# Kernel optimization log

Measured on AMD Instinct MI355X. Metric: run time of the kernel, lower is better.

The kernel has to match this reference:

```python
import jax, jax.numpy as jnp
import numpy as np

TOP_K = 2


def _mlp(x, w1, b1, w2, b2):
    # Linear -> GELU -> Linear (assumed MLP body)
    h = jax.nn.gelu(jnp.einsum('bsd,di->bsi', x, w1) + b1)
    return jnp.einsum('bsi,id->bsd', h, w2) + b2


def setup_inputs() -> dict:
    key = jax.random.key(0)
    ks = jax.random.split(key, 8)
    B, S, D, I, E = 2, 2048, 1024, 4096, 8
    s_in = 1.0 / np.sqrt(D)
    s_mid = 1.0 / np.sqrt(I)
    return {
        'x': jax.random.normal(ks[0], (B, S, D), jnp.float32),
        'gate_w': jax.random.normal(ks[1], (D, E), jnp.float32) * s_in,
        'gate_b': jnp.zeros((E,), jnp.float32),
        'sh_w1': jax.random.normal(ks[2], (D, I), jnp.float32) * s_in,
        'sh_b1': jnp.zeros((I,), jnp.float32),
        'sh_w2': jax.random.normal(ks[3], (I, D), jnp.float32) * s_mid,
        'sh_b2': jnp.zeros((D,), jnp.float32),
        'ew1': jax.random.normal(ks[4], (E, D, I), jnp.float32) * s_in,
        'eb1': jnp.zeros((E, I), jnp.float32),
        'ew2': jax.random.normal(ks[5], (E, I, D), jnp.float32) * s_mid,
        'eb2': jnp.zeros((E, D), jnp.float32),
    }


def reference(x, gate_w, gate_b, sh_w1, sh_b1, sh_w2, sh_b2, ew1, eb1, ew2, eb2):
    E = ew1.shape[0]
    # Router
    router_probs = jax.nn.softmax(jnp.einsum('bsd,de->bse', x, gate_w) + gate_b, axis=-1)
    expert_values, expert_indices = jax.lax.top_k(router_probs, k=TOP_K)  # (B,S,K)
    expert_values = expert_values / (jnp.sum(expert_values, axis=-1, keepdims=True) + 1e-9)
    # Dense compute of all experts (faithful to original)
    h = jax.nn.gelu(jnp.einsum('bsd,edi->bsei', x, ew1) + eb1)  # (B,S,E,I)
    all_outputs = jnp.einsum('bsei,eid->bsed', h, ew2) + eb2    # (B,S,E,D)
    # Combine: scatter top-k weights to dense (B,S,E) then weighted sum
    one_hot = jax.nn.one_hot(expert_indices, E, dtype=x.dtype)  # (B,S,K,E)
    weights_E = (one_hot * expert_values[..., None]).sum(axis=2)  # (B,S,E)
    moe_out = jnp.einsum('bse,bsed->bsd', weights_E, all_outputs)
    return x + _mlp(x, sh_w1, sh_b1, sh_w2, sh_b2) + moe_out
```

## Files before the change

kernel.cpp:

```cpp
#include <hip/hip_runtime.h>
#include <hip/hip_bf16.h>
#include <stdint.h>

typedef short bf16x8 __attribute__((ext_vector_type(8)));
typedef float f32x4  __attribute__((ext_vector_type(4)));
typedef unsigned short u16;

#define T_TOK 4096
#define D_DIM 1024
#define I_DIM 4096
#define NE    9
#define BK    32

__device__ __forceinline__ u16 f2bf(float f) {
    union { float f; uint32_t u; } v; v.f = f;
    uint32_t u = v.u;
    u += 0x7FFFu + ((u >> 16) & 1u);
    return (u16)(u >> 16);
}

__device__ __forceinline__ float gelu_fast(float v) {
    float c2 = 1.5957691216057308f * (v + 0.044715f * v * v * v);
    return v / (1.0f + __expf(-c2));
}

__device__ __forceinline__ void gl16(const void* g, void* l) {
    __builtin_amdgcn_global_load_lds(
        (const __attribute__((address_space(1))) void*)g,
        (__attribute__((address_space(3))) void*)l, 16, 0, 0);
}

#define DSR(dst, adr, IMM) \
    asm volatile("ds_read_b128 %0, %1 offset:" #IMM : "=v"(dst) : "v"(adr) : "memory")
#define WAIT_VM(N)  asm volatile("s_waitcnt vmcnt(" #N ")" ::: "memory")
#define WAIT_LGKM() asm volatile("s_waitcnt lgkmcnt(0)" ::: "memory")

__global__ void k_init(int* counts) {
    int i = threadIdx.x;
    if (i < 16) counts[i] = (i == 8) ? T_TOK : 0;
}

__global__ __launch_bounds__(256) void k_router(
    const float* __restrict__ x, const float* __restrict__ gw,
    const float* __restrict__ gb,
    int* counts, int* lists, int* tok_e, int* tok_pos, float* tok_w)
{
    int wave = threadIdx.x >> 6, lane = threadIdx.x & 63;
    int t = blockIdx.x * 4 + wave;
    const float* xr = x + (size_t)t * D_DIM;

    float a[8];
#pragma unroll
    for (int e = 0; e < 8; ++e) a[e] = 0.f;
#pragma unroll
    for (int j = 0; j < D_DIM / 64; ++j) {
        int d = lane + 64 * j;
        float xv = xr[d];
        const float4* g = (const float4*)(gw + (size_t)d * 8);
        float4 g0 = g[0], g1 = g[1];
        a[0] += xv * g0.x; a[1] += xv * g0.y; a[2] += xv * g0.z; a[3] += xv * g0.w;
        a[4] += xv * g1.x; a[5] += xv * g1.y; a[6] += xv * g1.z; a[7] += xv * g1.w;
    }
#pragma unroll
    for (int off = 32; off >= 1; off >>= 1)
#pragma unroll
        for (int e = 0; e < 8; ++e) a[e] += __shfl_xor(a[e], off);

    float l[8];
#pragma unroll
    for (int e = 0; e < 8; ++e) l[e] = a[e] + gb[e];
    float mx = l[0];
#pragma unroll
    for (int e = 1; e < 8; ++e) mx = fmaxf(mx, l[e]);
    float p[8], Z = 0.f;
#pragma unroll
    for (int e = 0; e < 8; ++e) { p[e] = expf(l[e] - mx); Z += p[e]; }
#pragma unroll
    for (int e = 0; e < 8; ++e) p[e] /= Z;

    int e0 = 0; float v0 = p[0];
#pragma unroll
    for (int e = 1; e < 8; ++e) if (p[e] > v0) { v0 = p[e]; e0 = e; }
    int e1 = -1; float v1 = -1.f;
#pragma unroll
    for (int e = 0; e < 8; ++e) if (e != e0 && p[e] > v1) { v1 = p[e]; e1 = e; }
    float denom = v0 + v1 + 1e-9f;
    float w0 = v0 / denom, w1 = v1 / denom;

    if (lane == 0) {
        int p0 = atomicAdd(&counts[e0], 1);
        int p1 = atomicAdd(&counts[e1], 1);
        lists[e0 * T_TOK + p0] = t;
        lists[e1 * T_TOK + p1] = t;
        tok_e[2 * t] = e0;  tok_e[2 * t + 1] = e1;
        tok_pos[2 * t] = p0; tok_pos[2 * t + 1] = p1;
        tok_w[2 * t] = w0;  tok_w[2 * t + 1] = w1;
    }
}

__global__ void k_prefix(const int* counts, int* offsets) {
    if (threadIdx.x == 0) {
        int o = 0;
        for (int e = 0; e < NE; ++e) { offsets[e] = o; o += counts[e]; }
        offsets[NE] = o;
    }
}

__global__ __launch_bounds__(256) void k_castx(const float* __restrict__ x,
                                               u16* __restrict__ xb)
{
    int i = (blockIdx.x * 256 + threadIdx.x) * 8;
    float4 a = *(const float4*)(x + i), b = *(const float4*)(x + i + 4);
    u16 t[8] = { f2bf(a.x), f2bf(a.y), f2bf(a.z), f2bf(a.w),
                 f2bf(b.x), f2bf(b.y), f2bf(b.z), f2bf(b.w) };
    *(bf16x8*)&xb[i] = *(bf16x8*)t;
}

__global__ __launch_bounds__(256) void k_transcast(
    const float* __restrict__ src, u16* __restrict__ dst, int K, int N)
{
    src += (size_t)blockIdx.z * K * N;
    dst += (size_t)blockIdx.z * N * K;
    __shared__ float ls[64][33];
    int t = threadIdx.x;
    int k0 = blockIdx.y * 64, n0 = blockIdx.x * 32;
    {
        int kr = t >> 2, ng = (t & 3) * 8;
        const float* s = src + (size_t)(k0 + kr) * N + n0 + ng;
        float4 v0 = *(const float4*)s, v1 = *(const float4*)(s + 4);
        ls[kr][ng + 0] = v0.x; ls[kr][ng + 1] = v0.y; ls[kr][ng + 2] = v0.z; ls[kr][ng + 3] = v0.w;
        ls[kr][ng + 4] = v1.x; ls[kr][ng + 5] = v1.y; ls[kr][ng + 6] = v1.z; ls[kr][ng + 7] = v1.w;
    }
    __syncthreads();
    int n = t >> 3, kg = (t & 7) * 8;
    u16 o[8];
#pragma unroll
    for (int j = 0; j < 8; ++j) o[j] = f2bf(ls[kg + j][n]);
    *(bf16x8*)&dst[(size_t)(n0 + n) * K + k0 + kg] = *(bf16x8*)o;
}

template <int GEMM>
__global__ __launch_bounds__(1024, 1)
void k_gemm(const u16* __restrict__ A, const u16* __restrict__ Bt,
            const float* __restrict__ be, const float* __restrict__ bsh,
            const int* __restrict__ counts, const int* __restrict__ offsets,
            const int* __restrict__ lists, void* __restrict__ Cg)
{
    constexpr int K   = (GEMM == 1) ? D_DIM : I_DIM;
    constexpr int N   = (GEMM == 1) ? I_DIM : D_DIM;
    constexpr int NT2 = N / 256;
    constexpr int G   = NE * NT2;
    constexpr int nk  = K / BK;

    const int bid = blockIdx.x;
    const int gi  = ((bid >> 3) >> 4) * 8 + (bid & 7);
    const int mt  = (bid >> 3) & 15;
    if (gi >= G) return;
    const int e = gi / NT2, nt = gi % NT2;
    const int cnt = counts[e];
    if (mt * 256 >= cnt) return;
    const int off = offsets[e];

    __shared__ __align__(16) u16 As0[8192], As1[8192];
    __shared__ __align__(16) u16 Bs0[8192], Bs1[8192];

    const int tid = threadIdx.x, w = tid >> 6, l = tid & 63;
    const int wu = __builtin_amdgcn_readfirstlane(w);
    const int wr = w >> 2, wc = w & 3;

    const int scol = ((l & 3) ^ ((l >> 3) & 3)) * 8;
    const int srow = w * 16 + (l >> 2);
    const uint32_t rch  = (uint32_t)(((l >> 4) ^ (((l & 15) >> 1) & 3)) << 4);
    const uint32_t aoff = (uint32_t)((wr * 64 + (l & 15)) * 64) + rch;
    const uint32_t boff = (uint32_t)((wc * 64 + (l & 15)) * 64) + rch;
    const uint32_t adr_a0 = (uint32_t)(uintptr_t)As0 + aoff;
    const uint32_t adr_a1 = (uint32_t)(uintptr_t)As1 + aoff;
    const uint32_t adr_b0 = (uint32_t)(uintptr_t)Bs0 + boff;
    const uint32_t adr_b1 = (uint32_t)(uintptr_t)Bs1 + boff;

    const u16* Be = Bt + (size_t)e * N * K;
    const u16* aptr;
    const u16* bptr;
    {
        int row = mt * 256 + srow;
        int sr;
        if constexpr (GEMM == 1) {
            if (e == 8) sr = row;
            else        sr = lists[e * T_TOK + (row < cnt ? row : cnt - 1)];
        } else {
            sr = off + row;
        }
        aptr = A + (size_t)sr * K + scol;
        bptr = Be + (size_t)(nt * 256 + srow) * K + scol;
    }

    f32x4 zero = {0.f, 0.f, 0.f, 0.f};
    f32x4 acc[4][4];
#pragma unroll
    for (int m = 0; m < 4; ++m)
#pragma unroll
        for (int n = 0; n < 4; ++n) acc[m][n] = zero;

    auto STG = [&](u16* Asb, u16* Bsb, int kt) {
        const int ko = kt * BK;
        gl16(aptr + ko, Asb + wu * 512);
        gl16(bptr + ko, Bsb + wu * 512);
    };
    auto RDM = [&](uint32_t aA, uint32_t aB, bool st, u16* sA, u16* sB, int knext) {
        bf16x8 fa[4], fb[4];
        DSR(fa[0], aA, 0);    DSR(fa[1], aA, 1024);
        DSR(fa[2], aA, 2048); DSR(fa[3], aA, 3072);
        DSR(fb[0], aB, 0);    DSR(fb[1], aB, 1024);
        DSR(fb[2], aB, 2048); DSR(fb[3], aB, 3072);
        WAIT_LGKM();
        __builtin_amdgcn_sched_barrier(0);
        __builtin_amdgcn_s_barrier();
        if (st) STG(sA, sB, knext);
        __builtin_amdgcn_s_setprio(1);
#pragma unroll
        for (int m = 0; m < 4; ++m)
#pragma unroll
            for (int n = 0; n < 4; ++n)
                acc[m][n] = __builtin_amdgcn_mfma_f32_16x16x32_bf16(fa[m], fb[n], acc[m][n], 0, 0, 0);
        __builtin_amdgcn_s_setprio(0);
    };

    STG(As0, Bs0, 0);
    STG(As1, Bs1, 1);
    for (int kt = 0; kt < nk - 2; kt += 2) {
        WAIT_VM(2);
        __builtin_amdgcn_s_barrier();
        RDM(adr_a0, adr_b0, true, As0, Bs0, kt + 2);
        WAIT_VM(2);
        __builtin_amdgcn_s_barrier();
        RDM(adr_a1, adr_b1, true, As1, Bs1, kt + 3);
    }
    WAIT_VM(2);
    __builtin_amdgcn_s_barrier();
    RDM(adr_a0, adr_b0, false, As0, Bs0, 0);
    WAIT_VM(0);
    __builtin_amdgcn_s_barrier();
    RDM(adr_a1, adr_b1, false, As1, Bs1, 0);

    const float* bias = (e == 8) ? bsh : (be + (size_t)e * N);
#pragma unroll
    for (int m = 0; m < 4; ++m) {
        int pbase = mt * 256 + wr * 64 + m * 16 + (l >> 4) * 4;
#pragma unroll
        for (int n = 0; n < 4; ++n) {
            int gcol = nt * 256 + wc * 64 + n * 16 + (l & 15);
            float bv = bias[gcol];
#pragma unroll
            for (int r = 0; r < 4; ++r) {
                int pos = pbase + r;
                if (pos < cnt) {
                    float v = acc[m][n][r] + bv;
                    if constexpr (GEMM == 1)
                        ((u16*)Cg)[(size_t)(off + pos) * N + gcol] = f2bf(gelu_fast(v));
                    else
                        ((float*)Cg)[(size_t)(off + pos) * N + gcol] = v;
                }
            }
        }
    }
}

__global__ __launch_bounds__(256) void k_combine(
    const float* __restrict__ x, const float* __restrict__ P,
    const int* __restrict__ offsets, const int* __restrict__ tok_e,
    const int* __restrict__ tok_pos, const float* __restrict__ tok_w,
    float* __restrict__ out)
{
    int t = blockIdx.x;
    int e0 = tok_e[2 * t], e1 = tok_e[2 * t + 1];
    int r0 = offsets[e0] + tok_pos[2 * t];
    int r1 = offsets[e1] + tok_pos[2 * t + 1];
    int rs = offsets[8] + t;
    float w0 = tok_w[2 * t], w1 = tok_w[2 * t + 1];
    int i = threadIdx.x * 4;

    float4 xv = *(const float4*)(x + (size_t)t * D_DIM + i);
    float4 ps = *(const float4*)(P + (size_t)rs * D_DIM + i);
    float4 p0 = *(const float4*)(P + (size_t)r0 * D_DIM + i);
    float4 p1 = *(const float4*)(P + (size_t)r1 * D_DIM + i);
    float4 o;
    o.x = xv.x + ps.x + w0 * p0.x + w1 * p1.x;
    o.y = xv.y + ps.y + w0 * p0.y + w1 * p1.y;
    o.z = xv.z + ps.z + w0 * p0.z + w1 * p1.z;
    o.w = xv.w + ps.w + w0 * p0.w + w1 * p1.w;
    *(float4*)(out + (size_t)t * D_DIM + i) = o;
}

extern "C" void kernel_launch(void* const* d_in, const int* in_sizes, int n_in,
                              void* d_out, int out_size, void* d_ws, size_t ws_size,
                              hipStream_t stream)
{
    const float* x   = (const float*)d_in[0];
    const float* gw  = (const float*)d_in[1];
    const float* gb  = (const float*)d_in[2];
    const float* sw1 = (const float*)d_in[3];
    const float* sb1 = (const float*)d_in[4];
    const float* sw2 = (const float*)d_in[5];
    const float* sb2 = (const float*)d_in[6];
    const float* ew1 = (const float*)d_in[7];
    const float* eb1 = (const float*)d_in[8];
    const float* ew2 = (const float*)d_in[9];
    const float* eb2 = (const float*)d_in[10];

    char* w = (char*)d_ws;
    int* counts  = (int*)w;
    int* offsets = (int*)(w + 64);
    int* tok_e   = (int*)(w + 2048);
    int* tok_pos = tok_e + 2 * T_TOK;
    float* tok_w = (float*)(tok_pos + 2 * T_TOK);
    int* lists   = (int*)(tok_w + 2 * T_TOK);

    size_t o = (size_t)1 << 20;
    u16* xb  = (u16*)(w + o);
    o += (size_t)T_TOK * D_DIM * 2;
    u16* H   = (u16*)(w + o);
    o += (size_t)3 * T_TOK * I_DIM * 2;
    u16* Wt  = (u16*)(w + o);
    o += (size_t)NE * I_DIM * D_DIM * 2;
    float* P = (float*)(w + o);

    k_init<<<1, 64, 0, stream>>>(counts);

    k_transcast<<<dim3(I_DIM / 32, D_DIM / 64, 8), 256, 0, stream>>>(ew1, Wt, D_DIM, I_DIM);
    k_transcast<<<dim3(I_DIM / 32, D_DIM / 64, 1), 256, 0, stream>>>(
        sw1, Wt + (size_t)8 * I_DIM * D_DIM, D_DIM, I_DIM);
    k_castx<<<T_TOK * D_DIM / (256 * 8), 256, 0, stream>>>(x, xb);

    k_router<<<T_TOK / 4, 256, 0, stream>>>(x, gw, gb, counts, lists, tok_e, tok_pos, tok_w);
    k_prefix<<<1, 64, 0, stream>>>(counts, offsets);

    k_gemm<1><<<144 * 16, 1024, 0, stream>>>(
        xb, Wt, eb1, sb1, counts, offsets, lists, (void*)H);

    k_transcast<<<dim3(D_DIM / 32, I_DIM / 64, 8), 256, 0, stream>>>(ew2, Wt, I_DIM, D_DIM);
    k_transcast<<<dim3(D_DIM / 32, I_DIM / 64, 1), 256, 0, stream>>>(
        sw2, Wt + (size_t)8 * I_DIM * D_DIM, I_DIM, D_DIM);

    k_gemm<2><<<40 * 16, 1024, 0, stream>>>(
        H, Wt, eb2, sb2, counts, offsets, lists, (void*)P);

    k_combine<<<T_TOK, 256, 0, stream>>>(x, P, offsets, tok_e, tok_pos, tok_w, (float*)d_out);
}
```

Before: 610.8 us.

## Use 4-stage LDS ring with 512-thread blocks and larger per-warp tiles in expert GEMMs

The expert GEMM kernel drops from 1024 to 512 threads per block, and each wave now computes a 128x64 output tile (8x4 MFMA tiles) instead of 64x64. The two-buffer double buffering is replaced by a four-slot LDS ring with a prefetch distance of three stages and one barrier per k-step. A and B global loads are split across the two MFMA halves so they interleave with compute. The aim is to hide memory latency better and reuse B fragments across twice as many A rows. The cost is a doubled accumulator register count and 128KB of LDS per block, which likely allows only one resident block per CU despite the launch bound requesting two.

```diff
diff --git a/kernel.cpp b/kernel.cpp
--- a/kernel.cpp
+++ b/kernel.cpp
@@ -140,7 +140,7 @@
 }
 
 template <int GEMM>
-__global__ __launch_bounds__(1024, 1)
+__global__ __launch_bounds__(512, 2)
 void k_gemm(const u16* __restrict__ A, const u16* __restrict__ Bt,
             const float* __restrict__ be, const float* __restrict__ bsh,
             const int* __restrict__ counts, const int* __restrict__ offsets,
@@ -161,28 +161,27 @@
     if (mt * 256 >= cnt) return;
     const int off = offsets[e];
 
-    __shared__ __align__(16) u16 As0[8192], As1[8192];
-    __shared__ __align__(16) u16 Bs0[8192], Bs1[8192];
+    __shared__ __align__(16) u16 AsAll[4 * 8192];
+    __shared__ __align__(16) u16 BsAll[4 * 8192];
 
     const int tid = threadIdx.x, w = tid >> 6, l = tid & 63;
     const int wu = __builtin_amdgcn_readfirstlane(w);
     const int wr = w >> 2, wc = w & 3;
 
     const int scol = ((l & 3) ^ ((l >> 3) & 3)) * 8;
-    const int srow = w * 16 + (l >> 2);
     const uint32_t rch  = (uint32_t)(((l >> 4) ^ (((l & 15) >> 1) & 3)) << 4);
-    const uint32_t aoff = (uint32_t)((wr * 64 + (l & 15)) * 64) + rch;
+    const uint32_t aoff = (uint32_t)((wr * 128 + (l & 15)) * 64) + rch;
     const uint32_t boff = (uint32_t)((wc * 64 + (l & 15)) * 64) + rch;
-    const uint32_t adr_a0 = (uint32_t)(uintptr_t)As0 + aoff;
-    const uint32_t adr_a1 = (uint32_t)(uintptr_t)As1 + aoff;
-    const uint32_t adr_b0 = (uint32_t)(uintptr_t)Bs0 + boff;
-    const uint32_t adr_b1 = (uint32_t)(uintptr_t)Bs1 + boff;
+    const uint32_t adr_a = (uint32_t)(uintptr_t)AsAll + aoff;
+    const uint32_t adr_b = (uint32_t)(uintptr_t)BsAll + boff;
 
     const u16* Be = Bt + (size_t)e * N * K;
-    const u16* aptr;
-    const u16* bptr;
-    {
-        int row = mt * 256 + srow;
+    const u16* aptr[2];
+    const u16* bptr[2];
+#pragma unroll
+    for (int j = 0; j < 2; ++j) {
+        int lr  = w * 32 + j * 16 + (l >> 2);
+        int row = mt * 256 + lr;
         int sr;
         if constexpr (GEMM == 1) {
             if (e == 8) sr = row;
@@ -190,32 +189,41 @@
         } else {
             sr = off + row;
         }
-        aptr = A + (size_t)sr * K + scol;
-        bptr = Be + (size_t)(nt * 256 + srow) * K + scol;
+        aptr[j] = A + (size_t)sr * K + scol;
+        bptr[j] = Be + (size_t)(nt * 256 + lr) * K + scol;
     }
 
     f32x4 zero = {0.f, 0.f, 0.f, 0.f};
-    f32x4 acc[4][4];
-#pragma unroll
-    for (int m = 0; m < 4; ++m)
+    f32x4 acc[8][4];
+#pragma unroll
+    for (int m = 0; m < 8; ++m)
 #pragma unroll
         for (int n = 0; n < 4; ++n) acc[m][n] = zero;
 
-    auto STG = [&](u16* Asb, u16* Bsb, int kt) {
-        const int ko = kt * BK;
-        gl16(aptr + ko, Asb + wu * 512);
-        gl16(bptr + ko, Bsb + wu * 512);
+    auto STG_A = [&](int s) {
+        u16* dst = AsAll + (s & 3) * 8192 + wu * 1024;
+        const int ko = s * BK;
+        gl16(aptr[0] + ko, dst);
+        gl16(aptr[1] + ko, dst + 512);
     };
-    auto RDM = [&](uint32_t aA, uint32_t aB, bool st, u16* sA, u16* sB, int knext) {
-        bf16x8 fa[4], fb[4];
+    auto STG_B = [&](int s) {
+        u16* dst = BsAll + (s & 3) * 8192 + wu * 1024;
+        const int ko = s * BK;
+        gl16(bptr[0] + ko, dst);
+        gl16(bptr[1] + ko, dst + 512);
+    };
+
+    auto STEP = [&](int s, bool st) {
+        const uint32_t aA = adr_a + (uint32_t)((s & 3) << 14);
+        const uint32_t aB = adr_b + (uint32_t)((s & 3) << 14);
+        bf16x8 fa[4], fb[4], ga[4];
         DSR(fa[0], aA, 0);    DSR(fa[1], aA, 1024);
         DSR(fa[2], aA, 2048); DSR(fa[3], aA, 3072);
         DSR(fb[0], aB, 0);    DSR(fb[1], aB, 1024);
         DSR(fb[2], aB, 2048); DSR(fb[3], aB, 3072);
+        if (st) STG_A(s + 3);
         WAIT_LGKM();
         __builtin_amdgcn_sched_barrier(0);
-        __builtin_amdgcn_s_barrier();
-        if (st) STG(sA, sB, knext);
         __builtin_amdgcn_s_setprio(1);
 #pragma unroll
         for (int m = 0; m < 4; ++m)
@@ -223,29 +231,34 @@
             for (int n = 0; n < 4; ++n)
                 acc[m][n] = __builtin_amdgcn_mfma_f32_16x16x32_bf16(fa[m], fb[n], acc[m][n], 0, 0, 0);
         __builtin_amdgcn_s_setprio(0);
+        DSR(ga[0], aA, 4096); DSR(ga[1], aA, 5120);
+        DSR(ga[2], aA, 6144); DSR(ga[3], aA, 7168);
+        if (st) STG_B(s + 3);
+        WAIT_LGKM();
+        __builtin_amdgcn_sched_barrier(0);
+        __builtin_amdgcn_s_setprio(1);
+#pragma unroll
+        for (int m = 0; m < 4; ++m)
+#pragma unroll
+            for (int n = 0; n < 4; ++n)
+                acc[4 + m][n] = __builtin_amdgcn_mfma_f32_16x16x32_bf16(ga[m], fb[n], acc[4 + m][n], 0, 0, 0);
+        __builtin_amdgcn_s_setprio(0);
     };
 
-    STG(As0, Bs0, 0);
-    STG(As1, Bs1, 1);
-    for (int kt = 0; kt < nk - 2; kt += 2) {
-        WAIT_VM(2);
+    STG_A(0); STG_B(0); STG_A(1); STG_B(1); STG_A(2); STG_B(2);
+    for (int s = 0; s < nk - 3; ++s) {
+        WAIT_VM(8);
         __builtin_amdgcn_s_barrier();
-        RDM(adr_a0, adr_b0, true, As0, Bs0, kt + 2);
-        WAIT_VM(2);
-        __builtin_amdgcn_s_barrier();
-        RDM(adr_a1, adr_b1, true, As1, Bs1, kt + 3);
-    }
-    WAIT_VM(2);
-    __builtin_amdgcn_s_barrier();
-    RDM(adr_a0, adr_b0, false, As0, Bs0, 0);
-    WAIT_VM(0);
-    __builtin_amdgcn_s_barrier();
-    RDM(adr_a1, adr_b1, false, As1, Bs1, 0);
+        STEP(s, true);
+    }
+    WAIT_VM(8); __builtin_amdgcn_s_barrier(); STEP(nk - 3, false);
+    WAIT_VM(4); __builtin_amdgcn_s_barrier(); STEP(nk - 2, false);
+    WAIT_VM(0); __builtin_amdgcn_s_barrier(); STEP(nk - 1, false);
 
     const float* bias = (e == 8) ? bsh : (be + (size_t)e * N);
 #pragma unroll
-    for (int m = 0; m < 4; ++m) {
-        int pbase = mt * 256 + wr * 64 + m * 16 + (l >> 4) * 4;
+    for (int m = 0; m < 8; ++m) {
+        int pbase = mt * 256 + wr * 128 + m * 16 + (l >> 4) * 4;
 #pragma unroll
         for (int n = 0; n < 4; ++n) {
             int gcol = nt * 256 + wc * 64 + n * 16 + (l & 15);
@@ -334,14 +347,14 @@
     k_router<<<T_TOK / 4, 256, 0, stream>>>(x, gw, gb, counts, lists, tok_e, tok_pos, tok_w);
     k_prefix<<<1, 64, 0, stream>>>(counts, offsets);
 
-    k_gemm<1><<<144 * 16, 1024, 0, stream>>>(
+    k_gemm<1><<<144 * 16, 512, 0, stream>>>(
         xb, Wt, eb1, sb1, counts, offsets, lists, (void*)H);
 
     k_transcast<<<dim3(D_DIM / 32, I_DIM / 64, 8), 256, 0, stream>>>(ew2, Wt, I_DIM, D_DIM);
     k_transcast<<<dim3(D_DIM / 32, I_DIM / 64, 1), 256, 0, stream>>>(
         sw2, Wt + (size_t)8 * I_DIM * D_DIM, I_DIM, D_DIM);
 
-    k_gemm<2><<<40 * 16, 1024, 0, stream>>>(
+    k_gemm<2><<<40 * 16, 512, 0, stream>>>(
         H, Wt, eb2, sb2, counts, offsets, lists, (void*)P);
 
     k_combine<<<T_TOK, 256, 0, stream>>>(x, P, offsets, tok_e, tok_pos, tok_w, (float*)d_out);
```

New measurement: 608.8 us. About the same (-0.3%).
